# Kernel tuning notes

Measured on AMD Instinct MI355X. Metric: run time of the kernel, lower is better.

Reference implementation:

```python
import jax, jax.numpy as jnp
import numpy as np

TRAIN_ROIS = 200
POS_RATIO = 0.33
POS_MAX = int(TRAIN_ROIS * POS_RATIO)  # 66
BBOX_STD = np.array([0.1, 0.1, 0.2, 0.2], dtype=np.float32)


def _iou(boxes1, boxes2):
    # boxes1 [N,4], boxes2 [G,4] in (y1,x1,y2,x2) -> IoU [N,G]
    b1 = boxes1[:, None, :]
    b2 = boxes2[None, :, :]
    y1 = jnp.maximum(b1[..., 0], b2[..., 0])
    x1 = jnp.maximum(b1[..., 1], b2[..., 1])
    y2 = jnp.minimum(b1[..., 2], b2[..., 2])
    x2 = jnp.minimum(b1[..., 3], b2[..., 3])
    inter = jnp.maximum(x2 - x1, 0.0) * jnp.maximum(y2 - y1, 0.0)
    a1 = (b1[..., 2] - b1[..., 0]) * (b1[..., 3] - b1[..., 1])
    a2 = (b2[..., 2] - b2[..., 0]) * (b2[..., 3] - b2[..., 1])
    union = a1 + a2 - inter
    return inter / jnp.where(union > 0, union, 1.0)


def _box_refine(box, gt):
    # standard Mask R-CNN box_refinement_graph
    h = box[..., 2] - box[..., 0]
    w = box[..., 3] - box[..., 1]
    cy = box[..., 0] + 0.5 * h
    cx = box[..., 1] + 0.5 * w
    gh = gt[..., 2] - gt[..., 0]
    gw = gt[..., 3] - gt[..., 1]
    gcy = gt[..., 0] + 0.5 * gh
    gcx = gt[..., 1] + 0.5 * gw
    return jnp.stack([(gcy - cy) / h, (gcx - cx) / w,
                      jnp.log(gh / h), jnp.log(gw / w)], axis=-1)


def _per_image(proposals, gt_boxes, gt_captions, scores):
    T = TRAIN_ROIS
    valid_p = jnp.sum(jnp.abs(proposals), axis=1) > 0   # trim_zeros on proposals
    valid_g = jnp.sum(jnp.abs(gt_boxes), axis=1) > 0    # trim_zeros on gt
    # IoU only feeds comparisons/argmax (pure index selection) -> no grad path
    overlaps = jax.lax.stop_gradient(_iou(proposals, gt_boxes))
    overlaps = jnp.where(valid_g[None, :], overlaps, -1.0)
    roi_iou_max = jnp.max(overlaps, axis=1)
    pos_bool = valid_p & (roi_iou_max >= 0.5)
    neg_bool = valid_p & (roi_iou_max < 0.5)
    # deterministic stand-in for tf.random.shuffle[:count]: first `count` in index order
    pos_idx = jnp.where(pos_bool, size=POS_MAX, fill_value=0)[0]
    pos_cnt = jnp.minimum(jnp.sum(pos_bool), POS_MAX)
    pos_valid = jnp.arange(POS_MAX) < pos_cnt
    neg_target = (pos_cnt.astype(jnp.float32) / POS_RATIO).astype(jnp.int32) - pos_cnt
    neg_idx = jnp.where(neg_bool, size=T, fill_value=0)[0]
    neg_cnt = jnp.minimum(jnp.minimum(neg_target, jnp.sum(neg_bool)), T - pos_cnt)
    neg_valid = jnp.arange(T) < neg_cnt

    positive_rois = proposals[pos_idx]                  # [POS_MAX,4]
    negative_rois = proposals[neg_idx]                  # [T,4]
    gt_assign = jnp.argmax(overlaps[pos_idx], axis=1)   # [POS_MAX]
    roi_gt_boxes = gt_boxes[gt_assign]
    roi_gt_captions = gt_captions[gt_assign]
    roi_gt_scores = scores[gt_assign]
    # for padded (invalid) positive slots, use the roi itself -> zero, finite deltas
    safe_gt = jnp.where(pos_valid[:, None], roi_gt_boxes, positive_rois)
    deltas = _box_refine(positive_rois, safe_gt) / jnp.asarray(BBOX_STD)

    # positives occupy slots [0,pos_cnt), negatives [pos_cnt, pos_cnt+neg_cnt), rest zero-padded
    pos_slots = jnp.where(pos_valid, jnp.arange(POS_MAX), T)   # T is out-of-range -> dropped
    neg_slots = jnp.where(neg_valid, pos_cnt + jnp.arange(T), T)
    rois = (jnp.zeros((T, 4), proposals.dtype)
            .at[pos_slots].set(positive_rois, mode='drop')
            .at[neg_slots].set(negative_rois, mode='drop'))
    out_deltas = jnp.zeros((T, 4), proposals.dtype).at[pos_slots].set(deltas, mode='drop')
    out_caps = jnp.zeros((T, gt_captions.shape[1]), gt_captions.dtype).at[pos_slots].set(roi_gt_captions, mode='drop')
    out_scores = jnp.zeros((T,), scores.dtype).at[pos_slots].set(roi_gt_scores, mode='drop')
    return rois, out_deltas, out_caps, out_scores


def setup_inputs() -> dict:
    key = jax.random.key(0)
    B, N, G = 8, 4096, 512
    k1, k2, k3, k4, k5 = jax.random.split(key, 5)
    c = jax.random.uniform(k1, (B, N, 2))                   # box centers (y,x)
    s = jax.random.uniform(k2, (B, N, 2)) * 0.2 + 0.02      # box sizes
    lo = jnp.clip(c - 0.5 * s, 0.0, 1.0)
    hi = jnp.clip(c + 0.5 * s, 0.0, 1.0)
    proposals = jnp.concatenate([lo, hi], axis=-1)          # (y1,x1,y2,x2)
    # gt boxes = perturbed copies of first G proposals (ensures IoU>=0.5 positives exist)
    p = proposals[:, :G, :] + jax.random.normal(k3, (B, G, 4)) * 0.02
    y1 = jnp.minimum(p[..., 0], p[..., 2]); y2 = jnp.maximum(p[..., 0], p[..., 2]) + 1e-3
    x1 = jnp.minimum(p[..., 1], p[..., 3]); x2 = jnp.maximum(p[..., 1], p[..., 3]) + 1e-3
    gt_boxes = jnp.clip(jnp.stack([y1, x1, y2, x2], axis=-1), 0.0, 1.0)
    # exercise the zero-trim logic: zero-pad tails
    proposals = proposals.at[:, N - 256:, :].set(0.0)
    gt_boxes = gt_boxes.at[:, G - 32:, :].set(0.0)
    gt_captions = jax.random.randint(k4, (B, G, 15), 0, 10000, dtype=jnp.int32)
    scores = jax.random.uniform(k5, (B, G))
    return {"proposals": proposals, "gt_boxes": gt_boxes,
            "gt_captions": gt_captions, "scores": scores}


def reference(proposals, gt_boxes, gt_captions, scores):
    return jax.vmap(_per_image)(proposals, gt_boxes, gt_captions, scores)
```

## Files before the change

kernel.cpp:

```cpp
#include <hip/hip_runtime.h>
#include <math.h>

#define BB   8
#define NP   4096
#define NG   512
#define TT   200
#define PMAX 66

#define CH   8
#define CSZ  64
#define PB   32

__global__ __launch_bounds__(256) void iou_phase(
    const float* __restrict__ proposals, const float* __restrict__ gt,
    int* __restrict__ argj, int* __restrict__ cls) {
#pragma clang fp contract(off)
  const int b     = blockIdx.x >> 7;
  const int pbase = (blockIdx.x & 127) * PB;

  __shared__ float4 sgt[NG];
  __shared__ float  sa2[NG];
  __shared__ float  sv[NG];
  __shared__ float  rbest[CH][PB];
  __shared__ int    ridx[CH][PB];

  const int tid = threadIdx.x;

  const float4* gtb4 = (const float4*)(gt + (size_t)b * NG * 4);
  for (int j = tid; j < NG; j += 256) {
    float4 g = gtb4[j];
    sgt[j] = g;
    sa2[j] = (g.z - g.x) * (g.w - g.y);
    sv[j]  = (fabsf(g.x) + fabsf(g.y) + fabsf(g.z) + fabsf(g.w)) > 0.0f ? 1.0f : 0.0f;
  }
  __syncthreads();

  const int plocal  = tid & (PB - 1);
  const int chunkid = tid >> 5;
  const int i       = pbase + plocal;
  const int jbase   = chunkid * CSZ;

  const float4 p = ((const float4*)(proposals))[(size_t)b * NP + i];
  const float p0 = p.x, p1 = p.y, p2 = p.z, p3 = p.w;
  const float a1 = (p2 - p0) * (p3 - p1);

  float best = -INFINITY;
  int bj = jbase;
  for (int jj = 0; jj < CSZ; ++jj) {
    int j = jbase + jj;
    float4 g = sgt[j];
    float y1 = fmaxf(p0, g.x);
    float x1 = fmaxf(p1, g.y);
    float y2 = fminf(p2, g.z);
    float x2 = fminf(p3, g.w);
    float inter = fmaxf(x2 - x1, 0.0f) * fmaxf(y2 - y1, 0.0f);
    float un = a1 + sa2[j] - inter;
    float iou = inter / (un > 0.0f ? un : 1.0f);
    float v = (sv[j] != 0.0f) ? iou : -1.0f;
    if (v > best) { best = v; bj = j; }
  }
  rbest[chunkid][plocal] = best;
  ridx[chunkid][plocal]  = bj;
  __syncthreads();

  if (tid < PB) {
    float bb = rbest[0][tid];
    int   bi = ridx[0][tid];
    for (int c = 1; c < CH; ++c) {
      float v = rbest[c][tid];
      if (v > bb) { bb = v; bi = ridx[c][tid]; }
    }
    bool vp = (fabsf(p0) + fabsf(p1) + fabsf(p2) + fabsf(p3)) > 0.0f;
    int c = vp ? (bb >= 0.5f ? 2 : 1) : 0;
    argj[(size_t)b * NP + i] = bi;
    cls[(size_t)b * NP + i]  = c;
  }
}

__global__ __launch_bounds__(256) void select_phase(
    const float* __restrict__ proposals, const float* __restrict__ gt,
    const int* __restrict__ caps, const float* __restrict__ scores,
    const int* __restrict__ argj, const int* __restrict__ cls,
    float* __restrict__ out) {
#pragma clang fp contract(off)
  const int b = blockIdx.x;

  __shared__ int s_posL[4][PMAX];
  __shared__ int s_negL[4][TT];
  __shared__ int s_pc[4], s_nc[4];

  const int tid  = threadIdx.x;
  const int w    = tid >> 6;
  const int lane = tid & 63;

  const int* clsb = cls + (size_t)b * NP;
  {
    int pcnt = 0, ncnt = 0;
    const int ibase = w * (NP / 4);
    for (int it = 0; it < NP / 4 / 64; ++it) {
      int i = ibase + it * 64 + lane;
      int c = clsb[i];
      unsigned long long mp = __ballot(c == 2);
      unsigned long long mn = __ballot(c == 1);
      unsigned long long lower = (1ull << lane) - 1ull;
      if (c == 2) {
        int k = pcnt + __popcll(mp & lower);
        if (k < PMAX) s_posL[w][k] = i;
      }
      if (c == 1) {
        int k = ncnt + __popcll(mn & lower);
        if (k < TT) s_negL[w][k] = i;
      }
      pcnt += __popcll(mp);
      ncnt += __popcll(mn);
    }
    if (lane == 0) { s_pc[w] = pcnt; s_nc[w] = ncnt; }
  }
  __syncthreads();

  const int pos_total = s_pc[0] + s_pc[1] + s_pc[2] + s_pc[3];
  const int neg_total = s_nc[0] + s_nc[1] + s_nc[2] + s_nc[3];
  int pos_cnt = pos_total < PMAX ? pos_total : PMAX;
  int neg_cnt = (int)((float)pos_cnt / 0.33f) - pos_cnt;
  if (neg_total < neg_cnt)    neg_cnt = neg_total;
  if (TT - pos_cnt < neg_cnt) neg_cnt = TT - pos_cnt;
  if (neg_cnt < 0)            neg_cnt = 0;

  float* rois   = out + (size_t)b * TT * 4;
  float* deltas = out + (size_t)BB * TT * 4 + (size_t)b * TT * 4;
  float* ocaps  = out + (size_t)2 * BB * TT * 4 + (size_t)b * TT * 15;
  float* osc    = out + (size_t)2 * BB * TT * 4 + (size_t)BB * TT * 15 + (size_t)b * TT;

  const int k = tid;
  if (k < TT) {
    if (k < pos_cnt) {
      int rem = k, w2 = 0;
      while (rem >= s_pc[w2]) { rem -= s_pc[w2]; ++w2; }
      int i = s_posL[w2][rem];

      const float* pp = proposals + ((size_t)b * NP + i) * 4;
      float p0 = pp[0], p1 = pp[1], p2 = pp[2], p3 = pp[3];
      int g = argj[(size_t)b * NP + i];
      const float* gg = gt + ((size_t)b * NG + g) * 4;
      float g0 = gg[0], g1 = gg[1], g2 = gg[2], g3 = gg[3];

      rois[k * 4 + 0] = p0; rois[k * 4 + 1] = p1;
      rois[k * 4 + 2] = p2; rois[k * 4 + 3] = p3;

      float h  = p2 - p0, ww = p3 - p1;
      float cy = p0 + 0.5f * h, cx = p1 + 0.5f * ww;
      float gh = g2 - g0, gw = g3 - g1;
      float gcy = g0 + 0.5f * gh, gcx = g1 + 0.5f * gw;
      deltas[k * 4 + 0] = ((gcy - cy) / h) / 0.1f;
      deltas[k * 4 + 1] = ((gcx - cx) / ww) / 0.1f;
      deltas[k * 4 + 2] = logf(gh / h) / 0.2f;
      deltas[k * 4 + 3] = logf(gw / ww) / 0.2f;

      const int* cp = caps + ((size_t)b * NG + g) * 15;
      for (int c = 0; c < 15; ++c) ocaps[k * 15 + c] = (float)cp[c];
      osc[k] = scores[(size_t)b * NG + g];
    } else {
      if (k < pos_cnt + neg_cnt) {
        int m = k - pos_cnt, w2 = 0;
        while (m >= s_nc[w2]) { m -= s_nc[w2]; ++w2; }
        int i = s_negL[w2][m];
        const float* pp = proposals + ((size_t)b * NP + i) * 4;
        rois[k * 4 + 0] = pp[0]; rois[k * 4 + 1] = pp[1];
        rois[k * 4 + 2] = pp[2]; rois[k * 4 + 3] = pp[3];
      } else {
        rois[k * 4 + 0] = 0.0f; rois[k * 4 + 1] = 0.0f;
        rois[k * 4 + 2] = 0.0f; rois[k * 4 + 3] = 0.0f;
      }
      deltas[k * 4 + 0] = 0.0f; deltas[k * 4 + 1] = 0.0f;
      deltas[k * 4 + 2] = 0.0f; deltas[k * 4 + 3] = 0.0f;
      for (int c = 0; c < 15; ++c) ocaps[k * 15 + c] = 0.0f;
      osc[k] = 0.0f;
    }
  }
}

extern "C" void kernel_launch(void* const* d_in, const int* in_sizes, int n_in,
                              void* d_out, int out_size, void* d_ws, size_t ws_size,
                              hipStream_t stream) {
  const float* proposals = (const float*)d_in[0];
  const float* gt        = (const float*)d_in[1];
  const int*   caps      = (const int*)d_in[2];
  const float* scores    = (const float*)d_in[3];
  float* out = (float*)d_out;

  int* argj = (int*)d_ws;
  int* cls  = (int*)((char*)d_ws + (size_t)BB * NP * sizeof(int));

  hipLaunchKernelGGL(iou_phase, dim3(BB * (NP / PB)), dim3(256), 0, stream,
                     proposals, gt, argj, cls);
  hipLaunchKernelGGL(select_phase, dim3(BB), dim3(256), 0, stream,
                     proposals, gt, caps, scores, argj, cls, out);
}
```

Baseline: 82.97 us.

## Compact valid GT boxes and pass per-block bitmasks to selection phase

The IoU kernel now compacts the non-zero ground-truth boxes into shared memory with a ballot-based prefix, so the inner loop only visits valid boxes and drops the per-iteration validity check. It also emits 32-bit positive and negative bitmasks per proposal block instead of a per-proposal class array. The select kernel then builds ordered index lists from those masks with a shared-memory scan, replacing a 4096-element serial scan over class values. The costs are a single-wavefront serial compaction at block start and the tie handling now depending on the compacted ordering.

```diff
diff --git a/kernel.cpp b/kernel.cpp
--- a/kernel.cpp
+++ b/kernel.cpp
@@ -8,56 +8,73 @@
 #define PMAX 66
 
 #define CH   8
-#define CSZ  64
 #define PB   32
+#define NBLK (NP / PB)
 
 __global__ __launch_bounds__(256) void iou_phase(
     const float* __restrict__ proposals, const float* __restrict__ gt,
-    int* __restrict__ argj, int* __restrict__ cls) {
+    int* __restrict__ argj, unsigned int* __restrict__ posmask,
+    unsigned int* __restrict__ negmask) {
 #pragma clang fp contract(off)
   const int b     = blockIdx.x >> 7;
-  const int pbase = (blockIdx.x & 127) * PB;
+  const int blk   = blockIdx.x & 127;
+  const int pbase = blk * PB;
 
   __shared__ float4 sgt[NG];
   __shared__ float  sa2[NG];
-  __shared__ float  sv[NG];
+  __shared__ short  sidx[NG];
+  __shared__ int    s_nv;
   __shared__ float  rbest[CH][PB];
   __shared__ int    ridx[CH][PB];
 
   const int tid = threadIdx.x;
 
-  const float4* gtb4 = (const float4*)(gt + (size_t)b * NG * 4);
-  for (int j = tid; j < NG; j += 256) {
-    float4 g = gtb4[j];
-    sgt[j] = g;
-    sa2[j] = (g.z - g.x) * (g.w - g.y);
-    sv[j]  = (fabsf(g.x) + fabsf(g.y) + fabsf(g.z) + fabsf(g.w)) > 0.0f ? 1.0f : 0.0f;
-  }
-  __syncthreads();
+  if (tid < 64) {
+    const float4* gtb4 = (const float4*)(gt + (size_t)b * NG * 4);
+    int cnt = 0;
+    for (int base = 0; base < NG; base += 64) {
+      int j = base + tid;
+      float4 g = gtb4[j];
+      bool v = (fabsf(g.x) + fabsf(g.y) + fabsf(g.z) + fabsf(g.w)) > 0.0f;
+      unsigned long long m = __ballot(v);
+      if (v) {
+        int k = cnt + __popcll(m & ((1ull << tid) - 1ull));
+        sgt[k]  = g;
+        sa2[k]  = (g.z - g.x) * (g.w - g.y);
+        sidx[k] = (short)j;
+      }
+      cnt += __popcll(m);
+    }
+    if (tid == 0) s_nv = cnt;
+  }
+  __syncthreads();
+
+  const int nv  = s_nv;
+  const int csz = (nv + CH - 1) / CH;
 
   const int plocal  = tid & (PB - 1);
   const int chunkid = tid >> 5;
   const int i       = pbase + plocal;
-  const int jbase   = chunkid * CSZ;
-
-  const float4 p = ((const float4*)(proposals))[(size_t)b * NP + i];
-  const float p0 = p.x, p1 = p.y, p2 = p.z, p3 = p.w;
-  const float a1 = (p2 - p0) * (p3 - p1);
+
+  const float4 p = ((const float4*)proposals)[(size_t)b * NP + i];
+  const float a1 = (p.z - p.x) * (p.w - p.y);
+
+  int j0 = chunkid * csz;
+  int j1 = j0 + csz; if (j1 > nv) j1 = nv;
+  if (j0 > nv) j0 = nv;
 
   float best = -INFINITY;
-  int bj = jbase;
-  for (int jj = 0; jj < CSZ; ++jj) {
-    int j = jbase + jj;
+  int bj = 0;
+  for (int j = j0; j < j1; ++j) {
     float4 g = sgt[j];
-    float y1 = fmaxf(p0, g.x);
-    float x1 = fmaxf(p1, g.y);
-    float y2 = fminf(p2, g.z);
-    float x2 = fminf(p3, g.w);
+    float y1 = fmaxf(p.x, g.x);
+    float x1 = fmaxf(p.y, g.y);
+    float y2 = fminf(p.z, g.z);
+    float x2 = fminf(p.w, g.w);
     float inter = fmaxf(x2 - x1, 0.0f) * fmaxf(y2 - y1, 0.0f);
     float un = a1 + sa2[j] - inter;
     float iou = inter / (un > 0.0f ? un : 1.0f);
-    float v = (sv[j] != 0.0f) ? iou : -1.0f;
-    if (v > best) { best = v; bj = j; }
+    if (iou > best) { best = iou; bj = (int)sidx[j]; }
   }
   rbest[chunkid][plocal] = best;
   ridx[chunkid][plocal]  = bj;
@@ -70,56 +87,75 @@
       float v = rbest[c][tid];
       if (v > bb) { bb = v; bi = ridx[c][tid]; }
     }
-    bool vp = (fabsf(p0) + fabsf(p1) + fabsf(p2) + fabsf(p3)) > 0.0f;
-    int c = vp ? (bb >= 0.5f ? 2 : 1) : 0;
+    bool vp  = (fabsf(p.x) + fabsf(p.y) + fabsf(p.z) + fabsf(p.w)) > 0.0f;
+    bool isp = vp && (bb >= 0.5f);
+    bool isn = vp && (bb <  0.5f);
+    unsigned long long mp = __ballot(isp);
+    unsigned long long mn = __ballot(isn);
     argj[(size_t)b * NP + i] = bi;
-    cls[(size_t)b * NP + i]  = c;
+    if (tid == 0) {
+      posmask[(size_t)b * NBLK + blk] = (unsigned int)mp;
+      negmask[(size_t)b * NBLK + blk] = (unsigned int)mn;
+    }
   }
 }
 
 __global__ __launch_bounds__(256) void select_phase(
     const float* __restrict__ proposals, const float* __restrict__ gt,
     const int* __restrict__ caps, const float* __restrict__ scores,
-    const int* __restrict__ argj, const int* __restrict__ cls,
-    float* __restrict__ out) {
+    const int* __restrict__ argj, const unsigned int* __restrict__ posmask,
+    const unsigned int* __restrict__ negmask, float* __restrict__ out) {
 #pragma clang fp contract(off)
   const int b = blockIdx.x;
 
-  __shared__ int s_posL[4][PMAX];
-  __shared__ int s_negL[4][TT];
-  __shared__ int s_pc[4], s_nc[4];
-
-  const int tid  = threadIdx.x;
-  const int w    = tid >> 6;
-  const int lane = tid & 63;
-
-  const int* clsb = cls + (size_t)b * NP;
-  {
-    int pcnt = 0, ncnt = 0;
-    const int ibase = w * (NP / 4);
-    for (int it = 0; it < NP / 4 / 64; ++it) {
-      int i = ibase + it * 64 + lane;
-      int c = clsb[i];
-      unsigned long long mp = __ballot(c == 2);
-      unsigned long long mn = __ballot(c == 1);
-      unsigned long long lower = (1ull << lane) - 1ull;
-      if (c == 2) {
-        int k = pcnt + __popcll(mp & lower);
-        if (k < PMAX) s_posL[w][k] = i;
-      }
-      if (c == 1) {
-        int k = ncnt + __popcll(mn & lower);
-        if (k < TT) s_negL[w][k] = i;
-      }
-      pcnt += __popcll(mp);
-      ncnt += __popcll(mn);
-    }
-    if (lane == 0) { s_pc[w] = pcnt; s_nc[w] = ncnt; }
-  }
-  __syncthreads();
-
-  const int pos_total = s_pc[0] + s_pc[1] + s_pc[2] + s_pc[3];
-  const int neg_total = s_nc[0] + s_nc[1] + s_nc[2] + s_nc[3];
+  __shared__ unsigned int s_pm[NBLK], s_nm[NBLK];
+  __shared__ int sc[256];
+  __shared__ int s_pos[PMAX];
+  __shared__ int s_neg[TT];
+
+  const int tid = threadIdx.x;
+  const int t   = tid & 127;
+
+  if (tid < NBLK) {
+    s_pm[tid] = posmask[(size_t)b * NBLK + tid];
+    s_nm[tid] = negmask[(size_t)b * NBLK + tid];
+  }
+  __syncthreads();
+
+  sc[tid] = (tid < 128) ? __popc(s_pm[t]) : __popc(s_nm[t]);
+  __syncthreads();
+  for (int off = 1; off < 128; off <<= 1) {
+    int v   = sc[tid];
+    int add = (t >= off) ? sc[tid - off] : 0;
+    __syncthreads();
+    sc[tid] = v + add;
+    __syncthreads();
+  }
+
+  const int pos_total = sc[127];
+  const int neg_total = sc[255];
+
+  if (tid < 128) {
+    unsigned int pm = s_pm[tid];
+    int base = (t == 0) ? 0 : sc[tid - 1];
+    while (pm && base < PMAX) {
+      int bit = __ffs(pm) - 1;
+      s_pos[base] = tid * PB + bit;
+      pm &= pm - 1;
+      ++base;
+    }
+  } else {
+    unsigned int nm = s_nm[t];
+    int base = (t == 0) ? 0 : sc[tid - 1];
+    while (nm && base < TT) {
+      int bit = __ffs(nm) - 1;
+      s_neg[base] = t * PB + bit;
+      nm &= nm - 1;
+      ++base;
+    }
+  }
+  __syncthreads();
+
   int pos_cnt = pos_total < PMAX ? pos_total : PMAX;
   int neg_cnt = (int)((float)pos_cnt / 0.33f) - pos_cnt;
   if (neg_total < neg_cnt)    neg_cnt = neg_total;
@@ -134,10 +170,7 @@
   const int k = tid;
   if (k < TT) {
     if (k < pos_cnt) {
-      int rem = k, w2 = 0;
-      while (rem >= s_pc[w2]) { rem -= s_pc[w2]; ++w2; }
-      int i = s_posL[w2][rem];
-
+      int i = s_pos[k];
       const float* pp = proposals + ((size_t)b * NP + i) * 4;
       float p0 = pp[0], p1 = pp[1], p2 = pp[2], p3 = pp[3];
       int g = argj[(size_t)b * NP + i];
@@ -161,9 +194,7 @@
       osc[k] = scores[(size_t)b * NG + g];
     } else {
       if (k < pos_cnt + neg_cnt) {
-        int m = k - pos_cnt, w2 = 0;
-        while (m >= s_nc[w2]) { m -= s_nc[w2]; ++w2; }
-        int i = s_negL[w2][m];
+        int i = s_neg[k - pos_cnt];
         const float* pp = proposals + ((size_t)b * NP + i) * 4;
         rois[k * 4 + 0] = pp[0]; rois[k * 4 + 1] = pp[1];
         rois[k * 4 + 2] = pp[2]; rois[k * 4 + 3] = pp[3];
@@ -188,11 +219,13 @@
   const float* scores    = (const float*)d_in[3];
   float* out = (float*)d_out;
 
-  int* argj = (int*)d_ws;
-  int* cls  = (int*)((char*)d_ws + (size_t)BB * NP * sizeof(int));
-
-  hipLaunchKernelGGL(iou_phase, dim3(BB * (NP / PB)), dim3(256), 0, stream,
-                     proposals, gt, argj, cls);
+  char* ws = (char*)d_ws;
+  int*          argj = (int*)ws;
+  unsigned int* pm   = (unsigned int*)(ws + (size_t)BB * NP * 4);
+  unsigned int* nm   = pm + (size_t)BB * NBLK;
+
+  hipLaunchKernelGGL(iou_phase, dim3(BB * NBLK), dim3(256), 0, stream,
+                     proposals, gt, argj, pm, nm);
   hipLaunchKernelGGL(select_phase, dim3(BB), dim3(256), 0, stream,
-                     proposals, gt, caps, scores, argj, cls, out);
+                     proposals, gt, caps, scores, argj, pm, nm, out);
 }
```

Result: no change. 81.48 us (-1.8%).
